# Kernel tuning notes

Measured on AMD Instinct MI355X. Metric: run time of the kernel, lower is better.

Reference implementation:

```python
import jax, jax.numpy as jnp
import numpy as np

D = 128           # volume / particle box size (pixels)
B = 8             # particles per batch
K = 125           # SO(3) grid poses (5x5x5 around each center Euler)
TOPK = 2          # keep_top_k_values
MAX_SHIFT_FRAC = 0.25  # main_config.projmatching.max_shift_fraction


def setup_inputs() -> dict:
    key = jax.random.key(0)
    k1, k2, k3, k4 = jax.random.split(key, 4)
    vol = jax.random.normal(k1, (D, D, D), dtype=jnp.float32)
    parts = jax.random.normal(k2, (B, D, D), dtype=jnp.float32)
    ctf = jax.random.uniform(k3, (B, D, D // 2 + 1), dtype=jnp.float32)
    euler_degs = jax.random.normal(k4, (K, 3), dtype=jnp.float32) * 8.0
    return {"vol": vol, "parts": parts, "ctf": ctf, "euler_degs": euler_degs}


def _rot_z(t):
    c, s = jnp.cos(t), jnp.sin(t)
    z, o = jnp.zeros_like(t), jnp.ones_like(t)
    return jnp.stack([jnp.stack([c, -s, z], -1),
                      jnp.stack([s, c, z], -1),
                      jnp.stack([z, z, o], -1)], -2)


def _rot_y(t):
    c, s = jnp.cos(t), jnp.sin(t)
    z, o = jnp.zeros_like(t), jnp.ones_like(t)
    return jnp.stack([jnp.stack([c, z, s], -1),
                      jnp.stack([z, o, z], -1),
                      jnp.stack([-s, z, c], -1)], -2)


def euler_zyz_to_matrix(degs):
    # RELION Euler convention ZYZ: R = Rz(a) @ Ry(b) @ Rz(c)
    rad = jnp.deg2rad(degs)
    return _rot_z(rad[..., 0]) @ _rot_y(rad[..., 1]) @ _rot_z(rad[..., 2])


def trilinear_sample(vol, zi, yi, xi):
    # vol: (Dz, Dy, W) complex64; coords: (K, h, w) float32 array indices
    Dz, Dy, W = vol.shape
    z0, y0, x0 = jnp.floor(zi), jnp.floor(yi), jnp.floor(xi)
    tz, ty, tx = zi - z0, yi - y0, xi - x0
    out = jnp.zeros(zi.shape, dtype=vol.dtype)
    for dz in (0, 1):
        wz = tz if dz else 1.0 - tz
        zc = z0 + dz
        vz = (zc >= 0) & (zc < Dz)
        zdx = jnp.clip(zc, 0, Dz - 1).astype(jnp.int32)
        for dy in (0, 1):
            wy = ty if dy else 1.0 - ty
            yc = y0 + dy
            vy = (yc >= 0) & (yc < Dy)
            ydx = jnp.clip(yc, 0, Dy - 1).astype(jnp.int32)
            for dx in (0, 1):
                wx = tx if dx else 1.0 - tx
                xc = x0 + dx
                vx = (xc >= 0) & (xc < W)
                xdx = jnp.clip(xc, 0, W - 1).astype(jnp.int32)
                w = jnp.where(vz & vy & vx, wz * wy * wx, 0.0)
                out = out + w * vol[zdx, ydx, xdx]
    return out


def project_fourier(vol_rfft, rotmats):
    # extract_central_slices_rfft: pose-dependent gather+trilinear interp of a
    # central slice from the fftshifted 3D rfft volume. Output: (K, D, D//2+1).
    d = D
    w = d // 2 + 1
    y = jnp.arange(d, dtype=jnp.float32) - d // 2   # fftshifted full-dim freqs (pixel units)
    x = jnp.arange(w, dtype=jnp.float32)            # rfft (non-negative) freqs
    yy, xx = jnp.meshgrid(y, x, indexing='ij')      # (d, w)
    coords = jnp.stack([xx, yy, jnp.zeros_like(yy)], -1)       # xyz, (d, w, 3), z = 0 plane
    rot = jnp.einsum('kij,hwj->khwi', rotmats, coords)          # (K, d, w, 3) rotated xyz
    conj_mask = rot[..., 0] < 0                                  # Hermitian symmetry: flip to x>=0 half
    rot = jnp.where(conj_mask[..., None], -rot, rot)
    xi = rot[..., 0]
    yi = rot[..., 1] + d // 2
    zi = rot[..., 2] + d // 2
    samples = trilinear_sample(vol_rfft, zi, yi, xi)
    samples = jnp.where(conj_mask, jnp.conj(samples), samples)
    r2 = xx ** 2 + yy ** 2                                       # zero beyond Nyquist radius
    samples = jnp.where(r2[None] > (d // 2) ** 2, 0.0, samples)
    return samples


def reference(vol, parts, ctf, euler_degs):
    # compute_dft: rfft volume, fftshift non-rfft dims
    vol_rfft = jnp.fft.fftshift(jnp.fft.rfftn(vol), axes=(0, 1))
    parts_rfft = jnp.fft.fftshift(jnp.fft.rfft2(parts), axes=(-2,))  # (B, D, W)
    rotmats = euler_zyz_to_matrix(euler_degs)                        # (K, 3, 3)
    projs = project_fourier(vol_rfft, rotmats)                       # (K, D, W)
    projs = ctf[:, None] * projs[None]                               # _apply_ctfF: (B, K, D, W)
    # correlate_dft_2d: cross-correlation via iFFT of parts * conj(projs)
    prod = parts_rfft[:, None] * jnp.conj(projs)
    prod = jnp.fft.ifftshift(prod, axes=(-2,))
    corr = jnp.fft.irfft2(prod, s=(D, D))                            # (B, K, D, D)
    corr = jnp.fft.fftshift(corr, axes=(-2, -1))                     # zero shift at center
    # _extract_ccor_max: restrict to |shift| <= max_shift_fraction*D, take top-k peaks
    center = D // 2
    max_shift = int(MAX_SHIFT_FRAC * D)
    idx = jnp.arange(D) - center
    win = (jnp.abs(idx)[:, None] <= max_shift) & (jnp.abs(idx)[None, :] <= max_shift)
    masked = jnp.where(win, corr, -jnp.inf)
    flat = masked.reshape(B, K, D * D)
    vals, top_idx = jax.lax.top_k(flat, TOPK)                        # (B, K, TOPK)
    shifts = jnp.stack([top_idx // D - center, top_idx % D - center], -1)  # (B, K, TOPK, 2) yx
    return vals, shifts
```

## Files before the change

### kernel.cpp

```cpp
#include <hip/hip_runtime.h>
#include <math.h>

#define D 128
#define W 65
#define NK 125
#define NB 8
#define SLAB (D*W)
#define TWO_PI 6.28318530717958647692f
#define R2C 0.70710678118654752440f
#define C8C 0.92387953251128675613f
#define S8C 0.38268343236508977173f
#define ARS 146
#define GS  67
#define BRS 68


__device__ __forceinline__ bool better(float va, int ia, float vb, int ib) {
    return (va > vb) || (va == vb && ia < ib);
}
__device__ __forceinline__ float2 cmul(float2 a, float2 b) {
    return make_float2(a.x*b.x - a.y*b.y, a.x*b.y + a.y*b.x);
}
__device__ __forceinline__ void cmac(float2& acc, float2 a, float2 b) {
    acc.x = fmaf(a.x, b.x, fmaf(-a.y, b.y, acc.x));
    acc.y = fmaf(a.x, b.y, fmaf( a.y, b.x, acc.y));
}
__device__ __forceinline__ float2 cadd(float2 a, float2 b){ return make_float2(a.x+b.x, a.y+b.y); }
__device__ __forceinline__ float2 csub(float2 a, float2 b){ return make_float2(a.x-b.x, a.y-b.y); }

__device__ __forceinline__ void fft8_fwd(const float2* x, float2* a) {
    float2 e0 = x[0], o0 = x[1], e1 = x[2], o1 = x[3];
    float2 e2 = x[4], o2 = x[5], e3 = x[6], o3 = x[7];
    float2 t0 = cadd(e0, e2), t1 = csub(e0, e2);
    float2 t2 = cadd(e1, e3), t3 = csub(e1, e3);
    float2 E0 = cadd(t0, t2), E2 = csub(t0, t2);
    float2 E1 = make_float2(t1.x + t3.y, t1.y - t3.x);
    float2 E3 = make_float2(t1.x - t3.y, t1.y + t3.x);
    float2 u0 = cadd(o0, o2), u1 = csub(o0, o2);
    float2 u2 = cadd(o1, o3), u3 = csub(o1, o3);
    float2 O0 = cadd(u0, u2), O2 = csub(u0, u2);
    float2 O1 = make_float2(u1.x + u3.y, u1.y - u3.x);
    float2 O3 = make_float2(u1.x - u3.y, u1.y + u3.x);
    float2 w1 = make_float2(R2C*(O1.x + O1.y), R2C*(O1.y - O1.x));
    float2 w2 = make_float2(O2.y, -O2.x);
    float2 w3 = make_float2(R2C*(O3.y - O3.x), -R2C*(O3.x + O3.y));
    a[0] = cadd(E0, O0); a[4] = csub(E0, O0);
    a[1] = cadd(E1, w1); a[5] = csub(E1, w1);
    a[2] = cadd(E2, w2); a[6] = csub(E2, w2);
    a[3] = cadd(E3, w3); a[7] = csub(E3, w3);
}

__device__ __forceinline__ void ifft8_reg(const float2* x, float2* a) {
    float2 e0 = x[0], o0 = x[1], e1 = x[2], o1 = x[3];
    float2 e2 = x[4], o2 = x[5], e3 = x[6], o3 = x[7];
    float2 t0 = cadd(e0, e2), t1 = csub(e0, e2);
    float2 t2 = cadd(e1, e3), t3 = csub(e1, e3);
    float2 E0 = cadd(t0, t2), E2 = csub(t0, t2);
    float2 E1 = make_float2(t1.x - t3.y, t1.y + t3.x);
    float2 E3 = make_float2(t1.x + t3.y, t1.y - t3.x);
    float2 u0 = cadd(o0, o2), u1 = csub(o0, o2);
    float2 u2 = cadd(o1, o3), u3 = csub(o1, o3);
    float2 O0 = cadd(u0, u2), O2 = csub(u0, u2);
    float2 O1 = make_float2(u1.x - u3.y, u1.y + u3.x);
    float2 O3 = make_float2(u1.x + u3.y, u1.y - u3.x);
    float2 w1o = make_float2(R2C*(O1.x - O1.y), R2C*(O1.x + O1.y));
    float2 w2o = make_float2(-O2.y, O2.x);
    float2 w3o = make_float2(R2C*(-O3.x - O3.y), R2C*(O3.x - O3.y));
    a[0] = cadd(E0, O0); a[4] = csub(E0, O0);
    a[1] = cadd(E1, w1o); a[5] = csub(E1, w1o);
    a[2] = cadd(E2, w2o); a[6] = csub(E2, w2o);
    a[3] = cadd(E3, w3o); a[7] = csub(E3, w3o);
}


template<int MODE>
__device__ __forceinline__ void fft128v2(const float* __restrict__ inf,
                                         const float2* __restrict__ inc,
                                         float2* __restrict__ out,
                                         const float* __restrict__ ct,
                                         int l0, int nlines,
                                         float2* __restrict__ Fl,
                                         float2* __restrict__ twf) {
    int tid = threadIdx.x;
    int line, t;
    if (MODE == 0) { t = tid & 7; line = tid >> 3; }
    else           { line = tid & 31; t = tid >> 5; }
    int l = l0 + line;
    bool live = (l < nlines);

    if (tid < 128) {
        float s, c;
        sincosf(-TWO_PI * (float)tid / 128.0f, &s, &c);
        twf[tid] = make_float2(c, s);
    }

    int base = 0, stride = 1;
    if (MODE == 1 || MODE == 4) { base = (l / W) * SLAB + (l % W); stride = W; }
    else if (MODE == 2) { base = l; stride = SLAB; }

    float2 xe[8], xo[8];
    if (live) {
        if (MODE == 0) {
            const float* r = inf + (size_t)l * D;
            #pragma unroll
            for (int j = 0; j < 8; ++j) {
                xe[j] = make_float2(r[t + 16*j], 0.f);
                xo[j] = make_float2(r[t + 8 + 16*j], 0.f);
            }
        } else {
            #pragma unroll
            for (int j = 0; j < 8; ++j) {
                xe[j] = inc[base + (t + 16*j) * stride];
                xo[j] = inc[base + (t + 8 + 16*j) * stride];
            }
        }
    } else {
        #pragma unroll
        for (int j = 0; j < 8; ++j) { xe[j] = make_float2(0,0); xo[j] = make_float2(0,0); }
    }
    float2 E[8], O[8];
    fft8_fwd(xe, E);
    fft8_fwd(xo, O);
    {
        const float2 w16[8] = {
            { 1.f, 0.f }, { C8C, -S8C }, { R2C, -R2C }, { S8C, -C8C },
            { 0.f, -1.f }, { -S8C, -C8C }, { -R2C, -R2C }, { -C8C, -S8C }
        };
        float2* Fp = Fl + line * 137 + t * 17;
        #pragma unroll
        for (int kk = 0; kk < 8; ++kk) {
            float2 wo = cmul(w16[kk], O[kk]);
            Fp[kk]     = cadd(E[kk], wo);
            Fp[kk + 8] = csub(E[kk], wo);
        }
    }
    __syncthreads();
    if (live) {
        const float2* Fr = Fl + line * 137;
        #pragma unroll
        for (int s = 0; s < 16; ++s) {
            int slot = t + 8 * s;
            if (MODE == 0 && slot > 64) break;
            int k = (MODE == 0) ? slot : (slot ^ 64);
            int kk = k & 15;
            float2 acc = make_float2(0.f, 0.f);
            #pragma unroll
            for (int tt = 0; tt < 8; ++tt) {
                cmac(acc, Fr[tt * 17 + kk], twf[(tt * k) & 127]);
            }
            if (MODE == 0)      out[(size_t)l * W + slot] = acc;
            else if (MODE == 4) {
                float cf = ct[(size_t)l * D + slot];
                out[(size_t)l * D + slot] = make_float2(acc.x * cf, acc.y * cf);
            }
            else                out[base + slot * stride] = acc;
        }
    }
}


__global__ __launch_bounds__(256) void k1_kernel(const float* __restrict__ vol,
                                                 const float* __restrict__ parts,
                                                 const float* __restrict__ ctf,
                                                 const float* __restrict__ euler,
                                                 float2* __restrict__ bufA,
                                                 float2* __restrict__ pT1,
                                                 float* __restrict__ CT,
                                                 float* __restrict__ rot) {
    __shared__ float2 Fl[32 * 137];
    __shared__ float2 twf[128];
    int bid = blockIdx.x;
    int tid = threadIdx.x;
    if (bid < 512) {
        fft128v2<0>(vol, nullptr, bufA, nullptr, bid * 32, D*D, Fl, twf);
    } else if (bid < 544) {
        fft128v2<0>(parts, nullptr, pT1, nullptr, (bid - 512) * 32, NB*D, Fl, twf);
    } else if (bid == 544) {
        int k = tid;
        if (k < NK) {
            const float d2r = 0.017453292519943295f;
            float a = euler[k*3+0]*d2r, b = euler[k*3+1]*d2r, c = euler[k*3+2]*d2r;
            float sa, ca, sb, cb, sc, cc;
            sincosf(a, &sa, &ca); sincosf(b, &sb, &cb); sincosf(c, &sc, &cc);
            rot[k*9+0] =  ca*cb*cc - sa*sc;
            rot[k*9+1] = -ca*cb*sc - sa*cc;
            rot[k*9+2] =  ca*sb;
            rot[k*9+3] =  sa*cb*cc + ca*sc;
            rot[k*9+4] = -sa*cb*sc + ca*cc;
            rot[k*9+5] =  sa*sb;
            rot[k*9+6] = -sb*cc;
            rot[k*9+7] =  sb*sc;
            rot[k*9+8] =  cb;
        }
    } else {
        int i = (bid - 545) * 256 + tid;
        if (i < NB * W * D) {
            int m = i & (D-1);
            int t2 = i >> 7;
            int x = t2 % W;
            int b = t2 / W;
            CT[i] = ctf[b * SLAB + m * W + x];
        }
    }
}

__global__ __launch_bounds__(256) void k2_kernel(const float2* __restrict__ bufA,
                                                 float2* __restrict__ bufB,
                                                 const float2* __restrict__ pT1,
                                                 float2* __restrict__ ST,
                                                 const float* __restrict__ CT) {
    __shared__ float2 Fl[32 * 137];
    __shared__ float2 twf[128];
    int bid = blockIdx.x;
    if (bid < 260) fft128v2<1>(nullptr, bufA, bufB, nullptr, bid * 32, D*W, Fl, twf);
    else           fft128v2<4>(nullptr, pT1, ST, CT, (bid - 260) * 32, NB*W, Fl, twf);
}

__global__ __launch_bounds__(256) void k3_kernel(const float2* __restrict__ bufB,
                                                 float2* __restrict__ bufA) {
    __shared__ float2 Fl[32 * 137];
    __shared__ float2 twf[128];
    fft128v2<2>(nullptr, bufB, bufA, nullptr, blockIdx.x * 32, SLAB, Fl, twf);
}


__global__ __launch_bounds__(256) void proj_kernel(const float2* __restrict__ vol,
                                                   const float* __restrict__ rot,
                                                   float2* __restrict__ projT) {
    int bid = blockIdx.x;
    int xcd = bid & 7, ii = bid >> 3;
    int wg = (xcd < 7) ? (xcd * 508 + ii) : (3556 + ii);
    int idx = wg * 256 + threadIdx.x;
    if (idx >= NK * D * W) return;
    int h = idx & (D-1);
    int t2 = idx >> 7;
    int w = t2 % W;
    int k = t2 / W;
    float x = (float)w;
    float y = (float)(h - 64);
    const float* R = rot + k*9;
    float rx = R[0]*x + R[1]*y;
    float ry = R[3]*x + R[4]*y;
    float rz = R[6]*x + R[7]*y;
    bool neg = rx < 0.0f;
    if (neg) { rx = -rx; ry = -ry; rz = -rz; }
    float xi = rx;
    float yi = ry + 64.0f;
    float zi = rz + 64.0f;
    float z0 = floorf(zi), y0 = floorf(yi), x0 = floorf(xi);
    float tz = zi - z0, ty = yi - y0, tx = xi - x0;
    int z0i = (int)z0, y0i = (int)y0, x0i = (int)x0;
    float ar = 0.f, ai = 0.f;
    for (int dz = 0; dz < 2; ++dz) {
        float wz = dz ? tz : 1.0f - tz;
        int zc = z0i + dz;
        bool vz = (zc >= 0) && (zc < D);
        int zx = min(max(zc, 0), D-1);
        for (int dy = 0; dy < 2; ++dy) {
            float wy = dy ? ty : 1.0f - ty;
            int yc = y0i + dy;
            bool vy = (yc >= 0) && (yc < D);
            int yx = min(max(yc, 0), D-1);
            for (int dx = 0; dx < 2; ++dx) {
                float wx = dx ? tx : 1.0f - tx;
                int xc = x0i + dx;
                bool vx = (xc >= 0) && (xc < W);
                int xx = min(max(xc, 0), W-1);
                float wt = (vz && vy && vx) ? wz*wy*wx : 0.0f;
                float2 v = vol[zx * SLAB + yx * W + xx];
                ar = fmaf(wt, v.x, ar);
                ai = fmaf(wt, v.y, ai);
            }
        }
    }
    if (neg) ai = -ai;
    int yy = h - 64;
    if (w*w + yy*yy > 4096) { ar = 0.f; ai = 0.f; }
    projT[idx] = make_float2(ar, ai);
}


__global__ __launch_bounds__(256, 2) void corr_kernel(const float2* __restrict__ ST,
                                                      const float2* __restrict__ PJT,
                                                      float* __restrict__ outv) {
    __shared__ float2 tw[128];
    __shared__ __align__(16) float2 AbBC[17*ARS];
    __shared__ float2 Gs[17*GS];
    __shared__ float  Ny[65];
    __shared__ float  redv[8];
    __shared__ int    redi[8];

    int g = blockIdx.x;
    int logical = (g & 7) * 125 + (g >> 3);
    int k = logical >> 3;
    int b = logical & 7;
    int tid = threadIdx.x;
    const float inv_d = 1.0f / 128.0f;

    if (tid < 128) {
        float s, c;
        sincosf(TWO_PI * (float)tid / 128.0f, &s, &c);
        tw[tid] = make_float2(c, s);
    }

    const float2* Sb = ST + b * (W * D);
    const float2* Jk = PJT + k * (W * D);

    int lane = tid & 63;
    int wv = tid >> 6;
    int sv = lane & 7;
    int vp = (96 + lane) & 127;
    float acc[16];
    #pragma unroll
    for (int j = 0; j < 16; ++j) acc[j] = 0.0f;
    float accR = 0.0f;
    int ur = 0, vr = 0;
    if (tid < 129) { if (tid < 65) { ur = 64; vr = tid; } else { ur = tid - 65; vr = 64; } }

    __syncthreads();

    float2 wvp = tw[vp];
    float2 tq = make_float2(1.0f, 0.0f);

    int l1 = tid >> 4, m01 = tid & 15;
    float2 Sv[8], Jv[8];
    float2 twr[8];
    twr[0] = make_float2(1.f, 0.f);
    #pragma unroll
    for (int r = 1; r < 8; ++r) twr[r] = tw[(r * m01) & 127];

    for (int cg = 0; cg < 4; ++cg) {
        if (cg == 0) {
            for (int i = tid; i < 17 * 16; i += 256) {
                int l = i >> 4, m0 = i & 15;
                int x = (l < 16) ? ((l >> 2) + 16 * (l & 3)) : 64;
                const float2* Sx = Sb + x * 128 + m0;
                const float2* Jx = Jk + x * 128 + m0;
                float2 p[8];
                #pragma unroll
                for (int j = 0; j < 8; ++j) {
                    float2 s = Sx[16*j];
                    float2 pj = Jx[16*j];
                    p[j] = make_float2(s.x*pj.x + s.y*pj.y, s.y*pj.x - s.x*pj.y);
                }
                float2 A[8];
                ifft8_reg(p, A);
                float2* dst = AbBC + l * ARS + m0;
                dst[0] = A[0];
                #pragma unroll
                for (int r = 1; r < 8; ++r) dst[r*18] = cmul(A[r], tw[(r * m0) & 127]);
            }
        } else {
            float2 p[8];
            #pragma unroll
            for (int j = 0; j < 8; ++j) {
                p[j] = make_float2(Sv[j].x*Jv[j].x + Sv[j].y*Jv[j].y,
                                   Sv[j].y*Jv[j].x - Sv[j].x*Jv[j].y);
            }
            float2 A[8];
            ifft8_reg(p, A);
            float2* dst = AbBC + l1 * ARS + m01;
            dst[0] = A[0];
            #pragma unroll
            for (int r = 1; r < 8; ++r) dst[r*18] = cmul(A[r], twr[r]);
        }
        if (cg < 3) {
            int xn = 4*(cg+1) + (l1 >> 2) + 16 * (l1 & 3);
            const float2* Sx = Sb + xn * 128 + m01;
            const float2* Jx = Jk + xn * 128 + m01;
            #pragma unroll
            for (int j = 0; j < 8; ++j) {
                Sv[j] = Sx[16*j];
                Jv[j] = Jx[16*j];
            }
        }
        __syncthreads();
        {
            int lim2 = (cg == 0) ? 136 : 128;
            for (int i = tid; i < lim2; i += 256) {
                int l, r;
                if (i < 128) { l = i & 15; r = i >> 4; }
                else         { l = 16; r = i - 128; }
                const float4* Ar = (const float4*)(AbBC + l * ARS + r * 18);
                float2 xe[8], xo[8];
                #pragma unroll
                for (int j = 0; j < 8; ++j) {
                    float4 a = Ar[j];
                    xe[j] = make_float2(a.x, a.y);
                    xo[j] = make_float2(a.z, a.w);
                }
                float2 E[8], O[8];
                ifft8_reg(xe, E);
                ifft8_reg(xo, O);
                const float2 w16p[8] = {
                    { 1.f, 0.f }, { C8C, S8C }, { R2C, R2C }, { S8C, C8C },
                    { 0.f, 1.f }, { -S8C, C8C }, { -R2C, R2C }, { -C8C, S8C }
                };
                float2* Gl = Gs + l * GS;
                #pragma unroll
                for (int t = 0; t < 8; ++t) {
                    float2 wo = cmul(w16p[t], O[t]);
                    float2 lowv  = cadd(E[t], wo);
                    float2 highv = csub(E[t], wo);
                    int klow = r + 8*t;
                    if (t <= 3) Gl[klow + 32] = lowv;
                    if (t == 4 && r == 0) Gl[64] = lowv;
                    if (t >= 4) Gl[klow - 32] = highv;
                }
            }
        }
        __syncthreads();
        {
            float2* BC = AbBC;
            int lim = (cg == 0) ? 325 : 260;
            for (int i = tid; i < lim; i += 256) {
                if (i < 260) {
                    int q = i / 65;
                    int u2 = i - q * 65;
                    float sg = (u2 & 1) ? -inv_d : inv_d;
                    const float2* Gq = Gs + (4*q) * GS + u2;
                    float2 h0 = Gq[0*GS];
                    float2 h1 = Gq[1*GS];
                    float2 h2 = Gq[2*GS];
                    float2 h3 = Gq[3*GS];
                    h0.x *= sg; h0.y *= sg; h1.x *= sg; h1.y *= sg;
                    h2.x *= sg; h2.y *= sg; h3.x *= sg; h3.y *= sg;
                    if (cg == 0 && q == 0) { h0.x *= 0.5f; h0.y *= 0.5f; }
                    const float sc = 2.0f * inv_d;
                    float2 p1 = make_float2(R2C*(h1.x - h1.y), R2C*(h1.x + h1.y));
                    float2 q1 = make_float2(R2C*(-h1.x - h1.y), R2C*(h1.x - h1.y));
                    float2 i1 = make_float2(-h1.y, h1.x);
                    float2 i2 = make_float2(-h2.y, h2.x);
                    float2 n2 = make_float2( h2.y, -h2.x);
                    float2 p3 = make_float2(R2C*(h3.x - h3.y), R2C*(h3.x + h3.y));
                    float2 q3 = make_float2(R2C*(-h3.x - h3.y), R2C*(h3.x - h3.y));
                    float2 i3 = make_float2(-h3.y, h3.x);
                    float2 a02 = cadd(h0, h2), s02 = csub(h0, h2);
                    float2 s0 = cadd(a02, cadd(h1, h3));
                    float2 s4 = csub(a02, cadd(h1, h3));
                    float2 s2 = cadd(s02, csub(i1, i3));
                    float2 s6 = csub(s02, csub(i1, i3));
                    float2 b0i = cadd(h0, i2);
                    float2 b0n = cadd(h0, n2);
                    float2 s1 = cadd(b0i, cadd(p1, q3));
                    float2 s5 = csub(b0i, cadd(p1, q3));
                    float2 s3 = cadd(b0n, cadd(q1, p3));
                    float2 s7 = csub(b0n, cadd(q1, p3));
                    float2* Bp = BC + q * (8*BRS) + u2;
                    Bp[0*BRS] = make_float2(s0.x*sc, s0.y*sc);
                    Bp[1*BRS] = make_float2(s1.x*sc, s1.y*sc);
                    Bp[2*BRS] = make_float2(s2.x*sc, s2.y*sc);
                    Bp[3*BRS] = make_float2(s3.x*sc, s3.y*sc);
                    Bp[4*BRS] = make_float2(s4.x*sc, s4.y*sc);
                    Bp[5*BRS] = make_float2(s5.x*sc, s5.y*sc);
                    Bp[6*BRS] = make_float2(s6.x*sc, s6.y*sc);
                    Bp[7*BRS] = make_float2(s7.x*sc, s7.y*sc);
                } else {
                    int u2 = i - 260;
                    Ny[u2] = ((u2 & 1) ? -inv_d : inv_d) * Gs[16*GS + u2].x;
                }
            }
        }
        __syncthreads();
        {
            #pragma unroll
            for (int q = 0; q < 4; ++q) {
                const float4* Bq = (const float4*)(AbBC + q * (8*BRS) + sv * BRS + wv * 16);
                float tx = tq.x, ty = tq.y;
                #pragma unroll
                for (int jp = 0; jp < 8; ++jp) {
                    float4 bb = Bq[jp];
                    acc[2*jp]   = fmaf(bb.x, tx, fmaf(-bb.y, ty, acc[2*jp]));
                    acc[2*jp+1] = fmaf(bb.z, tx, fmaf(-bb.w, ty, acc[2*jp+1]));
                }
                tq = cmul(tq, wvp);
            }
            if (cg == 0) {
                float sgn = (lane & 1) ? -inv_d : inv_d;
                #pragma unroll
                for (int j = 0; j < 16; ++j) acc[j] = fmaf(sgn, Ny[wv * 16 + j], acc[j]);
            }
            if (tid < 129) {
                int sr = vr & 7;
                int vpr = (96 + vr) & 127;
                float a = accR;
                #pragma unroll
                for (int q = 0; q < 4; ++q) {
                    float2 t = tw[((4*cg + q) * vpr) & 127];
                    float2 bv = AbBC[q * (8*BRS) + sr * BRS + ur];
                    a = fmaf(bv.x, t.x, fmaf(-bv.y, t.y, a));
                }
                if (cg == 0) a += (vr & 1) ? -inv_d * Ny[ur] : inv_d * Ny[ur];
                accR = a;
            }
        }
        __syncthreads();
    }

    float v1 = -INFINITY, v2 = -INFINITY;
    int i1 = 0x7fffffff, i2 = 0x7fffffff;
    #pragma unroll
    for (int j = 0; j < 16; ++j) {
        float val = acc[j];
        int uu = wv * 16 + j;
        int fl = (32 + uu) * D + (32 + lane);
        if (better(val, fl, v1, i1)) { v2 = v1; i2 = i1; v1 = val; i1 = fl; }
        else if (better(val, fl, v2, i2)) { v2 = val; i2 = fl; }
    }
    if (tid < 129) {
        int fl = (32 + ur) * D + (32 + vr);
        if (better(accR, fl, v1, i1)) { v2 = v1; i2 = i1; v1 = accR; i1 = fl; }
        else if (better(accR, fl, v2, i2)) { v2 = accR; i2 = fl; }
    }
    for (int off = 32; off > 0; off >>= 1) {
        float b1 = __shfl_down(v1, off); int j1 = __shfl_down(i1, off);
        float b2 = __shfl_down(v2, off); int j2 = __shfl_down(i2, off);
        if (better(b1, j1, v1, i1)) {
            float nv2; int ni2;
            if (better(v1, i1, b2, j2)) { nv2 = v1; ni2 = i1; } else { nv2 = b2; ni2 = j2; }
            v1 = b1; i1 = j1; v2 = nv2; i2 = ni2;
        } else {
            if (better(b1, j1, v2, i2)) { v2 = b1; i2 = j1; }
        }
    }
    int wave = tid >> 6;
    if ((tid & 63) == 0) {
        redv[wave*2]   = v1; redi[wave*2]   = i1;
        redv[wave*2+1] = v2; redi[wave*2+1] = i2;
    }
    __syncthreads();
    if (tid == 0) {
        float r1 = -INFINITY, r2 = -INFINITY;
        int q1 = 0x7fffffff, q2 = 0x7fffffff;
        for (int i = 0; i < 8; ++i) {
            float val = redv[i]; int fl = redi[i];
            if (better(val, fl, r1, q1)) { r2 = r1; q2 = q1; r1 = val; q1 = fl; }
            else if (better(val, fl, r2, q2)) { r2 = val; q2 = fl; }
        }
        int base = (b * NK + k) * 2;
        outv[base]     = r1;
        outv[base + 1] = r2;
        float* os = outv + NB*NK*2;
        os[(base    )*2 + 0] = (float)(q1 / D - 64);
        os[(base    )*2 + 1] = (float)(q1 % D - 64);
        os[(base + 1)*2 + 0] = (float)(q2 / D - 64);
        os[(base + 1)*2 + 1] = (float)(q2 % D - 64);
    }
}


extern "C" void kernel_launch(void* const* d_in, const int* in_sizes, int n_in,
                              void* d_out, int out_size, void* d_ws, size_t ws_size,
                              hipStream_t stream) {
    const float* vol   = (const float*)d_in[0];
    const float* parts = (const float*)d_in[1];
    const float* ctf   = (const float*)d_in[2];
    const float* euler = (const float*)d_in[3];
    float* out = (float*)d_out;

    const int VOLC = D * SLAB;
    float2* bufA   = (float2*)d_ws;
    float2* bufB   = bufA + VOLC;
    float2* pT1    = bufB + VOLC;
    float2* ST     = pT1 + NB * SLAB;
    float2* PJT    = ST + NB * W * D;
    float*  CT     = (float*)(PJT + NK * W * D);
    float*  rot    = CT + NB * W * D;

    k1_kernel<<<805, 256, 0, stream>>>(vol, parts, ctf, euler, bufA, pT1, CT, rot);
    k2_kernel<<<277, 256, 0, stream>>>(bufA, bufB, pT1, ST, CT);
    k3_kernel<<<260, 256, 0, stream>>>(bufB, bufA);
    proj_kernel<<<4063, 256, 0, stream>>>(bufA, rot, PJT);
    corr_kernel<<<NB * NK, 256, 0, stream>>>(ST, PJT, out);
}
```

Baseline: 82.05 us.

## Early-exit outside Fourier mask in projection; drop register prefetch, raise corr occupancy

In the projection kernel, threads whose frequency lies outside the radius-64 circle now write zero and return before the trilinear gather, so they skip eight global loads and the interpolation math. In the correlation kernel, the register-held prefetch of the next column group's spectra is removed and every group is loaded and transformed inside one uniform loop. Launch bounds go from 2 to 3 blocks per SIMD. Fewer registers per thread should allow more resident blocks to hide latency, at the cost of losing the explicit load-compute overlap.

Measured after the change: 78.22 us. -4.7%, faster.

```diff
diff --git a/kernel.cpp b/kernel.cpp
--- a/kernel.cpp
+++ b/kernel.cpp
@@ -236,8 +236,10 @@
     int t2 = idx >> 7;
     int w = t2 % W;
     int k = t2 / W;
+    int yy = h - 64;
+    if (w*w + yy*yy > 4096) { projT[idx] = make_float2(0.f, 0.f); return; }
     float x = (float)w;
-    float y = (float)(h - 64);
+    float y = (float)yy;
     const float* R = rot + k*9;
     float rx = R[0]*x + R[1]*y;
     float ry = R[3]*x + R[4]*y;
@@ -274,13 +276,11 @@
         }
     }
     if (neg) ai = -ai;
-    int yy = h - 64;
-    if (w*w + yy*yy > 4096) { ar = 0.f; ai = 0.f; }
     projT[idx] = make_float2(ar, ai);
 }
 
 
-__global__ __launch_bounds__(256, 2) void corr_kernel(const float2* __restrict__ ST,
+__global__ __launch_bounds__(256, 3) void corr_kernel(const float2* __restrict__ ST,
                                                       const float2* __restrict__ PJT,
                                                       float* __restrict__ outv) {
     __shared__ float2 tw[128];
@@ -322,18 +322,12 @@
     float2 wvp = tw[vp];
     float2 tq = make_float2(1.0f, 0.0f);
 
-    int l1 = tid >> 4, m01 = tid & 15;
-    float2 Sv[8], Jv[8];
-    float2 twr[8];
-    twr[0] = make_float2(1.f, 0.f);
-    #pragma unroll
-    for (int r = 1; r < 8; ++r) twr[r] = tw[(r * m01) & 127];
-
     for (int cg = 0; cg < 4; ++cg) {
-        if (cg == 0) {
-            for (int i = tid; i < 17 * 16; i += 256) {
+        {
+            int lim1 = (cg == 0) ? 17 * 16 : 16 * 16;
+            for (int i = tid; i < lim1; i += 256) {
                 int l = i >> 4, m0 = i & 15;
-                int x = (l < 16) ? ((l >> 2) + 16 * (l & 3)) : 64;
+                int x = (l < 16) ? (4*cg + (l >> 2) + 16 * (l & 3)) : 64;
                 const float2* Sx = Sb + x * 128 + m0;
                 const float2* Jx = Jk + x * 128 + m0;
                 float2 p[8];
@@ -349,29 +343,6 @@
                 dst[0] = A[0];
                 #pragma unroll
                 for (int r = 1; r < 8; ++r) dst[r*18] = cmul(A[r], tw[(r * m0) & 127]);
-            }
-        } else {
-            float2 p[8];
-            #pragma unroll
-            for (int j = 0; j < 8; ++j) {
-                p[j] = make_float2(Sv[j].x*Jv[j].x + Sv[j].y*Jv[j].y,
-                                   Sv[j].y*Jv[j].x - Sv[j].x*Jv[j].y);
-            }
-            float2 A[8];
-            ifft8_reg(p, A);
-            float2* dst = AbBC + l1 * ARS + m01;
-            dst[0] = A[0];
-            #pragma unroll
-            for (int r = 1; r < 8; ++r) dst[r*18] = cmul(A[r], twr[r]);
-        }
-        if (cg < 3) {
-            int xn = 4*(cg+1) + (l1 >> 2) + 16 * (l1 & 3);
-            const float2* Sx = Sb + xn * 128 + m01;
-            const float2* Jx = Jk + xn * 128 + m01;
-            #pragma unroll
-            for (int j = 0; j < 8; ++j) {
-                Sv[j] = Sx[16*j];
-                Jv[j] = Jx[16*j];
             }
         }
         __syncthreads();
```
